# Optimization experiments

Measured on AMD Instinct MI355X. Metric: run time of the kernel, lower is better.

Reference implementation:

```python
import jax, jax.numpy as jnp
import numpy as np

SEQ = 2048
D_MODEL = 2048
N_HEAD = 16
D_QK = 128
D_V = 128


def setup_inputs() -> dict:
    key = jax.random.key(0)
    ks = jax.random.split(key, 5)
    return {
        "x": jax.random.normal(ks[0], (SEQ, D_MODEL), dtype=jnp.float32),
        "q": jax.random.normal(ks[1], (N_HEAD, D_MODEL, D_QK), dtype=jnp.float32),
        "k": jax.random.normal(ks[2], (N_HEAD, D_MODEL, D_QK), dtype=jnp.float32),
        "v": jax.random.normal(ks[3], (N_HEAD, D_MODEL, D_V), dtype=jnp.float32),
        "o": jax.random.normal(ks[4], (N_HEAD, D_V, D_MODEL), dtype=jnp.float32),
        "theta_factor": jnp.asarray(10000.0, dtype=jnp.float32),
    }


def _rope_embed(x, theta_factor, d_qk):
    # x: [n_head, seq, d_qk]; faithful to source: rate is LINEAR in theta_factor
    seq = x.shape[1]
    d_rope = d_qk // 2
    rate = theta_factor * (-jnp.arange(d_rope, dtype=x.dtype) / d_rope)  # [d_rope]
    pos = jnp.arange(seq, dtype=x.dtype)                                 # [seq]
    rot = pos[:, None] * rate[None, :]                                   # [seq, d_rope]
    sin, cos = jnp.sin(rot), jnp.cos(rot)
    x1, x2 = x[..., :d_rope], x[..., d_rope:]
    y = jnp.concatenate([cos * x1 - sin * x2, sin * x1 + cos * x2], axis=-1)
    return y / d_qk ** 0.25  # qk_layer_norm is None path


def reference(x, q, k, v, o, theta_factor):
    seq, d_model = x.shape
    n_head, _, d_qk = q.shape
    d_v = v.shape[2]
    scale = 1.0 / jnp.sqrt(jnp.asarray(n_head * d_v * d_model, dtype=x.dtype))
    # causal mask: (tril - 1) * 1e9, as in source
    mask = (jnp.tril(jnp.ones((seq, seq), dtype=x.dtype)) - 1.0) * 1e9
    # per-head projections (vmapped heads expressed as einsum over h)
    rq = _rope_embed(jnp.einsum('sd,hde->hse', x, q), theta_factor, d_qk)
    rk = _rope_embed(jnp.einsum('sd,hde->hse', x, k), theta_factor, d_qk)
    vs = jnp.einsum('sd,hdv->hsv', x, v)
    scores = jnp.einsum('hse,hte->hst', rq, rk) + mask  # [h, s, s]
    w = jax.nn.softmax(scores, axis=-1)
    y = jnp.einsum('hst,htv->hsv', w, vs)
    z = jnp.einsum('hsv,hvd->sd', y, o)
    return z * scale
```

## Files before the change

kernel.cpp:

```cpp
#include <hip/hip_runtime.h>
#include <math.h>


typedef _Float16 half_t;
typedef __attribute__((ext_vector_type(8))) _Float16 half8;
typedef __attribute__((ext_vector_type(4))) float f32x4;

#define SEQ   2048
#define DM    2048
#define NHEAD 16

__device__ __forceinline__ f32x4 mfma16(half8 a, half8 b, f32x4 c) {
  return __builtin_amdgcn_mfma_f32_16x16x32_f16(a, b, c, 0, 0, 0);
}

__device__ __forceinline__ void gll16(const half_t* g, half_t* l) {
  __builtin_amdgcn_global_load_lds(
      (const __attribute__((address_space(1))) unsigned int*)g,
      (__attribute__((address_space(3))) unsigned int*)l, 16, 0, 0);
}

template <int CTRL>
__device__ __forceinline__ float dppf(float v) {
  int r = __builtin_amdgcn_mov_dpp(__builtin_bit_cast(int, v), CTRL, 0xF, 0xF,
                                   true);
  return __builtin_bit_cast(float, r);
}
__device__ __forceinline__ float red16_max(float v) {
  v = fmaxf(v, dppf<0xB1>(v));
  v = fmaxf(v, dppf<0x4E>(v));
  v = fmaxf(v, dppf<0x141>(v));
  v = fmaxf(v, dppf<0x140>(v));
  return v;
}
__device__ __forceinline__ float red16_sum(float v) {
  v += dppf<0xB1>(v);
  v += dppf<0x4E>(v);
  v += dppf<0x141>(v);
  v += dppf<0x140>(v);
  return v;
}

__global__ __launch_bounds__(256)
void k_split4(const float* __restrict__ in, half_t* __restrict__ hi,
              half_t* __restrict__ lo, int n4) {
  int i = blockIdx.x * 256 + threadIdx.x;
  if (i >= n4) return;
  float4 v = ((const float4*)in)[i];
  union { half_t h[4]; uint2 u; } H, L;
  H.h[0] = (half_t)v.x; H.h[1] = (half_t)v.y;
  H.h[2] = (half_t)v.z; H.h[3] = (half_t)v.w;
  L.h[0] = (half_t)(v.x - (float)H.h[0]);
  L.h[1] = (half_t)(v.y - (float)H.h[1]);
  L.h[2] = (half_t)(v.z - (float)H.h[2]);
  L.h[3] = (half_t)(v.w - (float)H.h[3]);
  *(uint2*)&hi[(size_t)i * 4] = H.u;
  *(uint2*)&lo[(size_t)i * 4] = L.u;
}

__global__ __launch_bounds__(256)
void k_transpose(const float* __restrict__ in, half_t* __restrict__ hi,
                 half_t* __restrict__ lo, int R, int C) {
  __shared__ float tile[32][33];
  size_t bo = (size_t)blockIdx.z * R * C;
  int c0 = blockIdx.x * 32, r0 = blockIdx.y * 32;
  int tx = threadIdx.x & 31, ty = threadIdx.x >> 5;
#pragma unroll
  for (int i = 0; i < 32; i += 8)
    tile[ty + i][tx] = in[bo + (size_t)(r0 + ty + i) * C + c0 + tx];
  __syncthreads();
#pragma unroll
  for (int i = 0; i < 32; i += 8) {
    float v = tile[tx][ty + i];
    half_t h = (half_t)v;
    size_t oidx = bo + (size_t)(c0 + ty + i) * R + r0 + tx;
    hi[oidx] = h;
    if (lo) lo[oidx] = (half_t)(v - (float)h);
  }
}

__device__ __forceinline__ int gemm_scol(int lane) {
  return (((lane & 3) ^ ((lane >> 3) & 3)) * 8);
}
__device__ __forceinline__ int gemm_fo(int row, int quad, int l15) {
  return row * 32 + ((quad ^ ((l15 >> 1) & 3)) * 8);
}

__global__ __launch_bounds__(256)
void k_proj(const half_t* __restrict__ Xh, const half_t* __restrict__ Xl,
            const half_t* __restrict__ WTh, const half_t* __restrict__ WTl,
            float* __restrict__ Craw) {
  __shared__ __align__(16) half_t sAh[128 * 32], sAl[128 * 32];
  __shared__ __align__(16) half_t sBh[128 * 32], sBl[128 * 32];
  int y = blockIdx.y;
  int m0 = blockIdx.x * 128;
  const half_t* wth = WTh + (size_t)y * 128 * DM;
  const half_t* wtl = WTl + (size_t)y * 128 * DM;
  int lane = threadIdx.x & 63, wave = threadIdx.x >> 6;
  int l15 = lane & 15, quad = lane >> 4;
  int wm = wave >> 1, wn = wave & 1;
  int srow = lane >> 2, scol = gemm_scol(lane);

  f32x4 acc[4][4];
#pragma unroll
  for (int a = 0; a < 4; ++a)
#pragma unroll
    for (int b = 0; b < 4; ++b) acc[a][b] = (f32x4)0.0f;

  for (int kt = 0; kt < DM / 32; ++kt) {
    int k0 = kt * 32;
#pragma unroll
    for (int i = 0; i < 2; ++i) {
      int c = wave * 2 + i;
      size_t ro = (size_t)(c * 16 + srow) * DM + k0 + scol;
      gll16(Xh + (size_t)m0 * DM + ro, sAh + c * 512);
      gll16(Xl + (size_t)m0 * DM + ro, sAl + c * 512);
      gll16(wth + ro, sBh + c * 512);
      gll16(wtl + ro, sBl + c * 512);
    }
    __syncthreads();
    half8 ah[4], al[4], bh[4], bl[4];
#pragma unroll
    for (int t = 0; t < 4; ++t) {
      int ao = gemm_fo(wm * 64 + t * 16 + l15, quad, l15);
      int bo = gemm_fo(wn * 64 + t * 16 + l15, quad, l15);
      ah[t] = *(const half8*)&sAh[ao];
      al[t] = *(const half8*)&sAl[ao];
      bh[t] = *(const half8*)&sBh[bo];
      bl[t] = *(const half8*)&sBl[bo];
    }
#pragma unroll
    for (int im = 0; im < 4; ++im)
#pragma unroll
      for (int in = 0; in < 4; ++in) {
        acc[im][in] = mfma16(ah[im], bh[in], acc[im][in]);
        acc[im][in] = mfma16(ah[im], bl[in], acc[im][in]);
        acc[im][in] = mfma16(al[im], bh[in], acc[im][in]);
      }
    __syncthreads();
  }
  float* cb = Craw + (size_t)y * SEQ * 128;
#pragma unroll
  for (int im = 0; im < 4; ++im)
#pragma unroll
    for (int in = 0; in < 4; ++in)
#pragma unroll
      for (int r = 0; r < 4; ++r) {
        int row = m0 + wm * 64 + im * 16 + quad * 4 + r;
        int col = wn * 64 + in * 16 + l15;
        cb[(size_t)row * 128 + col] = acc[im][in][r];
      }
}

__global__ __launch_bounds__(256)
void k_rope(const float* __restrict__ Craw, half_t* __restrict__ Rh,
            half_t* __restrict__ Rl, const float* __restrict__ thetap) {
  int which = blockIdx.z, h = blockIdx.y;
  int s = blockIdx.x * 4 + (threadIdx.x >> 6);
  int e = threadIdx.x & 63;
  float th = thetap[0];
  size_t base = ((size_t)(which * NHEAD + h) * SEQ + s) * 128;
  float x1 = Craw[base + e];
  float x2 = Craw[base + 64 + e];
  float rate = th * (-(float)e * (1.0f / 64.0f));
  float rot = (float)s * rate;
  float sn = sinf(rot), cs = cosf(rot);
  const float inv4 = 0.2973017787506803f;
  float y1 = (cs * x1 - sn * x2) * inv4;
  float y2 = (sn * x1 + cs * x2) * inv4;
  half_t h1 = (half_t)y1, h2 = (half_t)y2;
  Rh[base + e] = h1;       Rl[base + e] = (half_t)(y1 - (float)h1);
  Rh[base + 64 + e] = h2;  Rl[base + 64 + e] = (half_t)(y2 - (float)h2);
}

template <int HALF_OUT>
__global__ __launch_bounds__(256)
void k_gemm1(const half_t* __restrict__ A, const half_t* __restrict__ B,
             void* __restrict__ Cv, float scale) {
  __shared__ __align__(16) half_t sA[128 * 32], sB[128 * 32];
  int am0 = blockIdx.y * 128, bn0 = blockIdx.x * 128;
  int lane = threadIdx.x & 63, wave = threadIdx.x >> 6;
  int l15 = lane & 15, quad = lane >> 4;
  int wm = wave >> 1, wn = wave & 1;
  int srow = lane >> 2, scol = gemm_scol(lane);

  f32x4 acc[4][4];
#pragma unroll
  for (int a = 0; a < 4; ++a)
#pragma unroll
    for (int b = 0; b < 4; ++b) acc[a][b] = (f32x4)0.0f;

  for (int kt = 0; kt < DM / 32; ++kt) {
    int k0 = kt * 32;
#pragma unroll
    for (int i = 0; i < 2; ++i) {
      int c = wave * 2 + i;
      size_t ro = (size_t)(c * 16 + srow) * 2048 + k0 + scol;
      gll16(A + (size_t)am0 * 2048 + ro, sA + c * 512);
      gll16(B + (size_t)bn0 * 2048 + ro, sB + c * 512);
    }
    __syncthreads();
    half8 ah[4], bh[4];
#pragma unroll
    for (int t = 0; t < 4; ++t) {
      ah[t] = *(const half8*)&sA[gemm_fo(wm * 64 + t * 16 + l15, quad, l15)];
      bh[t] = *(const half8*)&sB[gemm_fo(wn * 64 + t * 16 + l15, quad, l15)];
    }
#pragma unroll
    for (int im = 0; im < 4; ++im)
#pragma unroll
      for (int in = 0; in < 4; ++in)
        acc[im][in] = mfma16(ah[im], bh[in], acc[im][in]);
    __syncthreads();
  }
#pragma unroll
  for (int im = 0; im < 4; ++im)
#pragma unroll
    for (int in = 0; in < 4; ++in)
#pragma unroll
      for (int r = 0; r < 4; ++r) {
        int row = am0 + wm * 64 + im * 16 + quad * 4 + r;
        int col = bn0 + wn * 64 + in * 16 + l15;
        if (HALF_OUT)
          ((half_t*)Cv)[(size_t)row * 2048 + col] = (half_t)(acc[im][in][r] * scale);
        else
          ((float*)Cv)[(size_t)row * 2048 + col] = acc[im][in][r] * scale;
      }
}

__global__ __launch_bounds__(256, 2)
void k_flash(const half_t* __restrict__ Rh, const half_t* __restrict__ Rl,
             const half_t* __restrict__ VST, half_t* __restrict__ Ybig) {
  int idx = blockIdx.x;
  int h = idx & 15;
  int qt = (idx < 256) ? (31 - (idx >> 4)) : ((idx - 256) >> 4);
  int lane = threadIdx.x & 63, wave = threadIdx.x >> 6;
  int l15 = lane & 15, quad = lane >> 4;

  const half_t* RQh = Rh + (size_t)h * SEQ * 128;
  const half_t* RQl = Rl + (size_t)h * SEQ * 128;
  const half_t* RKh = Rh + (size_t)(NHEAD + h) * SEQ * 128;
  const half_t* RKl = Rl + (size_t)(NHEAD + h) * SEQ * 128;
  const half_t* Vt  = VST + (size_t)h * 128 * SEQ;

  __shared__ __align__(16) half_t sKh[64 * 128];
  __shared__ __align__(16) half_t sKl[64 * 128];
  __shared__ __align__(16) half_t sVt[128 * 64];
  __shared__ __align__(16) half_t sP[64 * 72];

  int q0 = qt * 64;

  half8 qh[4], ql[4];
#pragma unroll
  for (int kk = 0; kk < 4; ++kk) {
    size_t ad = (size_t)(q0 + wave * 16 + l15) * 128 + kk * 32 + quad * 8;
    qh[kk] = *(const half8*)&RQh[ad];
    ql[kk] = *(const half8*)&RQl[ad];
  }

  float m_st[4], l_st[4];
  f32x4 oacc[8];
#pragma unroll
  for (int r = 0; r < 4; ++r) { m_st[r] = -INFINITY; l_st[r] = 0.0f; }
#pragma unroll
  for (int iv = 0; iv < 8; ++iv) oacc[iv] = (f32x4)0.0f;

  int nkb = qt + 1;
  for (int kb = 0; kb < nkb; ++kb) {
    int t0 = kb * 64;
#pragma unroll
    for (int i = 0; i < 4; ++i) {
      int c = wave * 4 + i;
      int rk = c * 4 + (lane >> 4);
      int ck = (lane & 15) ^ (rk & 15);
      gll16(RKh + (size_t)(t0 + rk) * 128 + ck * 8, sKh + c * 512);
      gll16(RKl + (size_t)(t0 + rk) * 128 + ck * 8, sKl + c * 512);
      int rv = c * 8 + (lane >> 3);
      int cv = (lane & 7) ^ (rv & 7);
      gll16(Vt + (size_t)rv * SEQ + t0 + cv * 8, sVt + c * 512);
    }
    __syncthreads();

    f32x4 sacc[4];
#pragma unroll
    for (int in = 0; in < 4; ++in) sacc[in] = (f32x4)0.0f;
#pragma unroll
    for (int kk = 0; kk < 4; ++kk)
#pragma unroll
      for (int in = 0; in < 4; ++in) {
        int bo = (in * 16 + l15) * 128 + (((kk * 4 + quad) ^ l15) * 8);
        half8 bh = *(const half8*)&sKh[bo];
        half8 bl = *(const half8*)&sKl[bo];
        sacc[in] = mfma16(qh[kk], bh, sacc[in]);
        sacc[in] = mfma16(qh[kk], bl, sacc[in]);
        sacc[in] = mfma16(ql[kk], bh, sacc[in]);
      }
    if (kb == qt) {
#pragma unroll
      for (int in = 0; in < 4; ++in)
#pragma unroll
        for (int r = 0; r < 4; ++r)
          if (in * 16 + l15 > wave * 16 + quad * 4 + r) sacc[in][r] = -1e30f;
    }
    float alpha[4];
#pragma unroll
    for (int r = 0; r < 4; ++r) {
      float mx = fmaxf(fmaxf(sacc[0][r], sacc[1][r]),
                       fmaxf(sacc[2][r], sacc[3][r]));
      mx = red16_max(mx);
      float mnew = fmaxf(m_st[r], mx);
      alpha[r] = __expf(m_st[r] - mnew);
      float sum = 0.0f;
#pragma unroll
      for (int in = 0; in < 4; ++in) {
        float p = __expf(sacc[in][r] - mnew);
        sacc[in][r] = p;
        sum += p;
      }
      sum = red16_sum(sum);
      l_st[r] = l_st[r] * alpha[r] + sum;
      m_st[r] = mnew;
    }
#pragma unroll
    for (int in = 0; in < 4; ++in)
#pragma unroll
      for (int r = 0; r < 4; ++r)
        sP[(wave * 16 + quad * 4 + r) * 72 + in * 16 + l15] =
            (half_t)sacc[in][r];
#pragma unroll
    for (int iv = 0; iv < 8; ++iv)
#pragma unroll
      for (int r = 0; r < 4; ++r) oacc[iv][r] *= alpha[r];

#pragma unroll
    for (int kk2 = 0; kk2 < 2; ++kk2) {
      half8 pa =
          *(const half8*)&sP[(wave * 16 + l15) * 72 + kk2 * 32 + quad * 8];
#pragma unroll
      for (int iv = 0; iv < 8; ++iv) {
        half8 vb = *(const half8*)&sVt[(iv * 16 + l15) * 64 +
                                       (((kk2 * 4 + quad) ^ (l15 & 7)) * 8)];
        oacc[iv] = mfma16(pa, vb, oacc[iv]);
      }
    }
    __syncthreads();
  }
  float invl[4];
#pragma unroll
  for (int r = 0; r < 4; ++r) invl[r] = 1.0f / l_st[r];
#pragma unroll
  for (int iv = 0; iv < 8; ++iv)
#pragma unroll
    for (int r = 0; r < 4; ++r) {
      int row = q0 + wave * 16 + quad * 4 + r;
      int col = h * 128 + iv * 16 + l15;
      Ybig[(size_t)row * 2048 + col] = (half_t)(oacc[iv][r] * invl[r]);
    }
}

extern "C" void kernel_launch(void* const* d_in, const int* in_sizes, int n_in,
                              void* d_out, int out_size, void* d_ws,
                              size_t ws_size, hipStream_t stream) {
  const float* x = (const float*)d_in[0];
  const float* q = (const float*)d_in[1];
  const float* k = (const float*)d_in[2];
  const float* v = (const float*)d_in[3];
  const float* o = (const float*)d_in[4];
  const float* theta = (const float*)d_in[5];
  float* out = (float*)d_out;

  char* ws = (char*)d_ws;
  const size_t HB = (size_t)2048 * 2048 * 2;
  half_t* Xh  = (half_t*)(ws);
  half_t* Xl  = (half_t*)(ws + HB);
  half_t* WTh = (half_t*)(ws + 2 * HB);
  half_t* WTl = (half_t*)(ws + 4 * HB);
  half_t* VhT = (half_t*)(ws + 6 * HB);
  half_t* OT  = (half_t*)(ws + 7 * HB);
  float*  Craw = (float*)(ws + 8 * HB);
  half_t* Rh = WTh;
  half_t* Rl = WTl;
  half_t* VST  = (half_t*)(ws + 8 * HB);
  half_t* Ybig = (half_t*)(ws + 9 * HB);

  k_split4<<<4096, 256, 0, stream>>>(x, Xh, Xl, (2048 * 2048) / 4);
  k_transpose<<<dim3(4, 64, 16), 256, 0, stream>>>(q, WTh, WTl, 2048, 128);
  k_transpose<<<dim3(4, 64, 16), 256, 0, stream>>>(
      k, WTh + (size_t)16 * 128 * 2048, WTl + (size_t)16 * 128 * 2048, 2048, 128);
  k_transpose<<<dim3(4, 64, 16), 256, 0, stream>>>(v, VhT, nullptr, 2048, 128);
  k_transpose<<<dim3(64, 64, 1), 256, 0, stream>>>(o, OT, nullptr, 2048, 2048);
  k_proj<<<dim3(16, 32), 256, 0, stream>>>(Xh, Xl, WTh, WTl, Craw);
  k_rope<<<dim3(512, 16, 2), 256, 0, stream>>>(Craw, Rh, Rl, theta);
  k_gemm1<1><<<dim3(16, 16), 256, 0, stream>>>(VhT, Xh, VST, 1.0f);
  k_flash<<<512, 256, 0, stream>>>(Rh, Rl, VST, Ybig);
  k_gemm1<0><<<dim3(16, 16), 256, 0, stream>>>(Ybig, OT, out, 1.0f / 2048.0f);
}
```

Measured before the change: 413.5 us.

## Double GEMM K-tile to 64 with XOR swizzle; amortize rope sin/cos across heads

The projection and generic GEMM kernels now stage 64-wide K tiles in LDS with an 8-way XOR swizzle, which halves the number of barrier-synchronised iterations. k_proj also gets a launch_bounds occupancy hint. The rope kernel now computes sin/cos once per (position, dim) and loops over all 32 head/which slices, and it range-reduces the angle in double precision first. The costs are more LDS per block (which may lower occupancy) and a sequential loop in rope over fewer blocks.

```diff
diff --git a/kernel.cpp b/kernel.cpp
--- a/kernel.cpp
+++ b/kernel.cpp
@@ -79,19 +79,13 @@
   }
 }
 
-__device__ __forceinline__ int gemm_scol(int lane) {
-  return (((lane & 3) ^ ((lane >> 3) & 3)) * 8);
-}
-__device__ __forceinline__ int gemm_fo(int row, int quad, int l15) {
-  return row * 32 + ((quad ^ ((l15 >> 1) & 3)) * 8);
-}
-
-__global__ __launch_bounds__(256)
+
+__global__ __launch_bounds__(256, 2)
 void k_proj(const half_t* __restrict__ Xh, const half_t* __restrict__ Xl,
             const half_t* __restrict__ WTh, const half_t* __restrict__ WTl,
             float* __restrict__ Craw) {
-  __shared__ __align__(16) half_t sAh[128 * 32], sAl[128 * 32];
-  __shared__ __align__(16) half_t sBh[128 * 32], sBl[128 * 32];
+  __shared__ __align__(16) half_t sAh[128 * 64], sAl[128 * 64];
+  __shared__ __align__(16) half_t sBh[128 * 64], sBl[128 * 64];
   int y = blockIdx.y;
   int m0 = blockIdx.x * 128;
   const half_t* wth = WTh + (size_t)y * 128 * DM;
@@ -99,7 +93,6 @@
   int lane = threadIdx.x & 63, wave = threadIdx.x >> 6;
   int l15 = lane & 15, quad = lane >> 4;
   int wm = wave >> 1, wn = wave & 1;
-  int srow = lane >> 2, scol = gemm_scol(lane);
 
   f32x4 acc[4][4];
 #pragma unroll
@@ -107,36 +100,44 @@
 #pragma unroll
     for (int b = 0; b < 4; ++b) acc[a][b] = (f32x4)0.0f;
 
-  for (int kt = 0; kt < DM / 32; ++kt) {
-    int k0 = kt * 32;
-#pragma unroll
-    for (int i = 0; i < 2; ++i) {
-      int c = wave * 2 + i;
-      size_t ro = (size_t)(c * 16 + srow) * DM + k0 + scol;
+  for (int kt = 0; kt < DM / 64; ++kt) {
+    int k0 = kt * 64;
+#pragma unroll
+    for (int i = 0; i < 4; ++i) {
+      int c = wave * 4 + i;
+      int g = c * 64 + lane;
+      int row = g >> 3;
+      int lc = (g & 7) ^ (row & 7);
+      size_t ro = (size_t)row * DM + k0 + lc * 8;
       gll16(Xh + (size_t)m0 * DM + ro, sAh + c * 512);
       gll16(Xl + (size_t)m0 * DM + ro, sAl + c * 512);
       gll16(wth + ro, sBh + c * 512);
       gll16(wtl + ro, sBl + c * 512);
     }
     __syncthreads();
-    half8 ah[4], al[4], bh[4], bl[4];
-#pragma unroll
-    for (int t = 0; t < 4; ++t) {
-      int ao = gemm_fo(wm * 64 + t * 16 + l15, quad, l15);
-      int bo = gemm_fo(wn * 64 + t * 16 + l15, quad, l15);
-      ah[t] = *(const half8*)&sAh[ao];
-      al[t] = *(const half8*)&sAl[ao];
-      bh[t] = *(const half8*)&sBh[bo];
-      bl[t] = *(const half8*)&sBl[bo];
-    }
-#pragma unroll
-    for (int im = 0; im < 4; ++im)
-#pragma unroll
-      for (int in = 0; in < 4; ++in) {
-        acc[im][in] = mfma16(ah[im], bh[in], acc[im][in]);
-        acc[im][in] = mfma16(ah[im], bl[in], acc[im][in]);
-        acc[im][in] = mfma16(al[im], bh[in], acc[im][in]);
-      }
+#pragma unroll
+    for (int kk = 0; kk < 2; ++kk) {
+      half8 ah[4], al[4], bh[4], bl[4];
+#pragma unroll
+      for (int t = 0; t < 4; ++t) {
+        int ar = wm * 64 + t * 16 + l15;
+        int br = wn * 64 + t * 16 + l15;
+        int ao = ar * 64 + (((kk * 4 + quad) ^ (ar & 7)) * 8);
+        int bo = br * 64 + (((kk * 4 + quad) ^ (br & 7)) * 8);
+        ah[t] = *(const half8*)&sAh[ao];
+        al[t] = *(const half8*)&sAl[ao];
+        bh[t] = *(const half8*)&sBh[bo];
+        bl[t] = *(const half8*)&sBl[bo];
+      }
+#pragma unroll
+      for (int im = 0; im < 4; ++im)
+#pragma unroll
+        for (int in = 0; in < 4; ++in) {
+          acc[im][in] = mfma16(ah[im], bh[in], acc[im][in]);
+          acc[im][in] = mfma16(ah[im], bl[in], acc[im][in]);
+          acc[im][in] = mfma16(al[im], bh[in], acc[im][in]);
+        }
+    }
     __syncthreads();
   }
   float* cb = Craw + (size_t)y * SEQ * 128;
@@ -155,34 +156,39 @@
 __global__ __launch_bounds__(256)
 void k_rope(const float* __restrict__ Craw, half_t* __restrict__ Rh,
             half_t* __restrict__ Rl, const float* __restrict__ thetap) {
-  int which = blockIdx.z, h = blockIdx.y;
-  int s = blockIdx.x * 4 + (threadIdx.x >> 6);
-  int e = threadIdx.x & 63;
+  int e = threadIdx.x & 63, sl = threadIdx.x >> 6;
+  int s = blockIdx.x * 4 + sl;
   float th = thetap[0];
-  size_t base = ((size_t)(which * NHEAD + h) * SEQ + s) * 128;
-  float x1 = Craw[base + e];
-  float x2 = Craw[base + 64 + e];
   float rate = th * (-(float)e * (1.0f / 64.0f));
   float rot = (float)s * rate;
-  float sn = sinf(rot), cs = cosf(rot);
+  double rev = (double)rot * 0.15915494309189535;
+  double fr = rev - rint(rev);
+  float thr = (float)(fr * 6.283185307179586);
+  float sn = sinf(thr), cs = cosf(thr);
   const float inv4 = 0.2973017787506803f;
-  float y1 = (cs * x1 - sn * x2) * inv4;
-  float y2 = (sn * x1 + cs * x2) * inv4;
-  half_t h1 = (half_t)y1, h2 = (half_t)y2;
-  Rh[base + e] = h1;       Rl[base + e] = (half_t)(y1 - (float)h1);
-  Rh[base + 64 + e] = h2;  Rl[base + 64 + e] = (half_t)(y2 - (float)h2);
+  float csn = cs * inv4, snn = sn * inv4;
+#pragma unroll 4
+  for (int y = 0; y < 32; ++y) {
+    size_t base = ((size_t)y * SEQ + s) * 128;
+    float x1 = Craw[base + e];
+    float x2 = Craw[base + 64 + e];
+    float y1 = csn * x1 - snn * x2;
+    float y2 = snn * x1 + csn * x2;
+    half_t h1 = (half_t)y1, h2 = (half_t)y2;
+    Rh[base + e] = h1;       Rl[base + e] = (half_t)(y1 - (float)h1);
+    Rh[base + 64 + e] = h2;  Rl[base + 64 + e] = (half_t)(y2 - (float)h2);
+  }
 }
 
 template <int HALF_OUT>
 __global__ __launch_bounds__(256)
 void k_gemm1(const half_t* __restrict__ A, const half_t* __restrict__ B,
              void* __restrict__ Cv, float scale) {
-  __shared__ __align__(16) half_t sA[128 * 32], sB[128 * 32];
+  __shared__ __align__(16) half_t sA[128 * 64], sB[128 * 64];
   int am0 = blockIdx.y * 128, bn0 = blockIdx.x * 128;
   int lane = threadIdx.x & 63, wave = threadIdx.x >> 6;
   int l15 = lane & 15, quad = lane >> 4;
   int wm = wave >> 1, wn = wave & 1;
-  int srow = lane >> 2, scol = gemm_scol(lane);
 
   f32x4 acc[4][4];
 #pragma unroll
@@ -190,27 +196,35 @@
 #pragma unroll
     for (int b = 0; b < 4; ++b) acc[a][b] = (f32x4)0.0f;
 
-  for (int kt = 0; kt < DM / 32; ++kt) {
-    int k0 = kt * 32;
-#pragma unroll
-    for (int i = 0; i < 2; ++i) {
-      int c = wave * 2 + i;
-      size_t ro = (size_t)(c * 16 + srow) * 2048 + k0 + scol;
+  for (int kt = 0; kt < DM / 64; ++kt) {
+    int k0 = kt * 64;
+#pragma unroll
+    for (int i = 0; i < 4; ++i) {
+      int c = wave * 4 + i;
+      int g = c * 64 + lane;
+      int row = g >> 3;
+      int lc = (g & 7) ^ (row & 7);
+      size_t ro = (size_t)row * 2048 + k0 + lc * 8;
       gll16(A + (size_t)am0 * 2048 + ro, sA + c * 512);
       gll16(B + (size_t)bn0 * 2048 + ro, sB + c * 512);
     }
     __syncthreads();
-    half8 ah[4], bh[4];
-#pragma unroll
-    for (int t = 0; t < 4; ++t) {
-      ah[t] = *(const half8*)&sA[gemm_fo(wm * 64 + t * 16 + l15, quad, l15)];
-      bh[t] = *(const half8*)&sB[gemm_fo(wn * 64 + t * 16 + l15, quad, l15)];
-    }
-#pragma unroll
-    for (int im = 0; im < 4; ++im)
-#pragma unroll
-      for (int in = 0; in < 4; ++in)
-        acc[im][in] = mfma16(ah[im], bh[in], acc[im][in]);
+#pragma unroll
+    for (int kk = 0; kk < 2; ++kk) {
+      half8 ah[4], bh[4];
+#pragma unroll
+      for (int t = 0; t < 4; ++t) {
+        int ar = wm * 64 + t * 16 + l15;
+        int br = wn * 64 + t * 16 + l15;
+        ah[t] = *(const half8*)&sA[ar * 64 + (((kk * 4 + quad) ^ (ar & 7)) * 8)];
+        bh[t] = *(const half8*)&sB[br * 64 + (((kk * 4 + quad) ^ (br & 7)) * 8)];
+      }
+#pragma unroll
+      for (int im = 0; im < 4; ++im)
+#pragma unroll
+        for (int in = 0; in < 4; ++in)
+          acc[im][in] = mfma16(ah[im], bh[in], acc[im][in]);
+    }
     __syncthreads();
   }
 #pragma unroll
@@ -390,7 +404,7 @@
   k_transpose<<<dim3(4, 64, 16), 256, 0, stream>>>(v, VhT, nullptr, 2048, 128);
   k_transpose<<<dim3(64, 64, 1), 256, 0, stream>>>(o, OT, nullptr, 2048, 2048);
   k_proj<<<dim3(16, 32), 256, 0, stream>>>(Xh, Xl, WTh, WTl, Craw);
-  k_rope<<<dim3(512, 16, 2), 256, 0, stream>>>(Craw, Rh, Rl, theta);
+  k_rope<<<512, 256, 0, stream>>>(Craw, Rh, Rl, theta);
   k_gemm1<1><<<dim3(16, 16), 256, 0, stream>>>(VhT, Xh, VST, 1.0f);
   k_flash<<<512, 256, 0, stream>>>(Rh, Rl, VST, Ybig);
   k_gemm1<0><<<dim3(16, 16), 256, 0, stream>>>(Ybig, OT, out, 1.0f / 2048.0f);
```

New measurement: 380.9 us. 7.9% less time.
